# Performance work log

Hardware: AMD Instinct MI355X
Metric: run time of the kernel (lower is better)

The kernel has to match this reference:

```python
import jax, jax.numpy as jnp
import numpy as np

N = 100000      # nodes
D = 128         # in_channels
P = 64          # num_prompts
E = 3_200_000   # graph edges
EPT = 5_000_000 # kNN prompt-graph edges (k=50)
EPS = 0.1       # ot_epsilon
ITERS = 20      # sinkhorn max_iters


def _l2norm(x):
    # F.normalize(p=2, dim=1) with eps=1e-12
    return x / jnp.maximum(jnp.linalg.norm(x, axis=1, keepdims=True), 1e-12)


def setup_inputs() -> dict:
    key = jax.random.key(0)
    k1, k2, k3, k4, k5 = jax.random.split(key, 5)
    x = jax.random.normal(k1, (N, D), dtype=jnp.float32)
    edge_index = jax.random.randint(k2, (2, E), 0, N, dtype=jnp.int32)
    edge_weight = jax.random.uniform(k3, (E,), dtype=jnp.float32)
    pt_edge_index = jax.random.randint(k4, (2, EPT), 0, N, dtype=jnp.int32)
    # xavier_uniform for prompt_tokens
    bound = float(np.sqrt(6.0 / (P + D)))
    prompt_tokens = jax.random.uniform(k5, (P, D), dtype=jnp.float32, minval=-bound, maxval=bound)
    alpha_feat = jnp.float32(0.01)
    gamma = jnp.float32(0.5)
    return {"x": x, "edge_index": edge_index, "edge_weight": edge_weight,
            "pt_edge_index": pt_edge_index, "prompt_tokens": prompt_tokens,
            "alpha_feat": alpha_feat, "gamma": gamma}


def reference(x, edge_index, edge_weight, pt_edge_index, prompt_tokens, alpha_feat, gamma):
    n = x.shape[0]
    row, col = edge_index[0], edge_index[1]
    # degree of col (unweighted count), GCN-style symmetric normalization
    deg = jax.ops.segment_sum(jnp.ones_like(edge_weight), col, num_segments=n)
    deg_inv_sqrt = jnp.where(deg > 0, deg ** -0.5, 0.0)
    norm_weight = deg_inv_sqrt[row] * edge_weight * deg_inv_sqrt[col]  # [E]
    # scatter-add aggregation: x_aggr[row] += x[col] * norm_weight
    x_aggr = jax.ops.segment_sum(x[col] * norm_weight[:, None], row, num_segments=n)
    x_struct = (1.0 - gamma) * x + gamma * x_aggr

    xs = _l2norm(x_struct)               # [N, D]
    pn = _l2norm(prompt_tokens)          # [P, D]

    # Sinkhorn OT: cost = 1 - cosine sim, uniform marginals
    C = 1.0 - xs @ pn.T                  # [N, P]
    K = jnp.exp(-C / EPS)
    p = prompt_tokens.shape[0]
    a = jnp.full((n,), 1.0 / n, dtype=x.dtype)
    b = jnp.full((p,), 1.0 / p, dtype=x.dtype)
    u = a
    for _ in range(ITERS):
        v = b / (K.T @ u + 1e-30)
        u = a / (K @ v + 1e-30)
    T_star = u[:, None] * K * v[None, :]  # [N, P]
    ot_loss = jnp.sum(T_star * C)

    prompt_message = n * (T_star @ prompt_tokens)  # [N, D]
    x_adapted = x + alpha_feat * prompt_message

    xf = _l2norm(x_adapted)
    pt_row, pt_col = pt_edge_index[0], pt_edge_index[1]
    w = jnp.sum(xf[pt_row] * xf[pt_col], axis=1)   # [EPT]
    w = jax.nn.relu(w)
    w = w / (jnp.max(w) + 1e-8)
    return (x_adapted, ot_loss, w)
```

## Files before the change

kernel.cpp:

```cpp
#include <hip/hip_runtime.h>
#include <stdint.h>

#define D_DIM 128
#define P_DIM 64

#define O_CNTR   0x000000ull
#define O_CNTC   0x080000ull
#define O_DIS    0x100000ull
#define O_ROWPTR 0x180000ull
#define O_CURSOR 0x200000ull
#define O_PART   0x280000ull
#define O_KT     0x290000ull
#define O_MAXW   0x2A0000ull
#define O_PNB    0x2B0000ull
#define O_U      0x300000ull
#define O_CSR    0x400000ull
#define O_XF     0x400000ull
#define O_K      0x1C80000ull
#define O_XB     0x3580000ull

__device__ __forceinline__ float wsumf(float v){
  #pragma unroll
  for (int d=1; d<64; d<<=1) v += __shfl_xor(v, d);
  return v;
}

__device__ __forceinline__ unsigned f2bf(float f){
  unsigned u = __float_as_uint(f);
  return (u + 0x7fffu + ((u>>16)&1u)) >> 16;
}

__device__ __forceinline__ float bflo(unsigned u){ return __uint_as_float(u<<16); }
__device__ __forceinline__ float bfhi(unsigned u){ return __uint_as_float(u & 0xffff0000u); }

__device__ __forceinline__ float dp2(unsigned a, unsigned b){
  return bflo(a)*bflo(b) + bfhi(a)*bfhi(b);
}

__global__ void k_zero(int* cntr, int* cntc, float* kt, unsigned* maxw, float* loss_slot, int n){
  int i = blockIdx.x*blockDim.x + threadIdx.x;
  int st = gridDim.x*blockDim.x;
  for (int j=i; j<n; j+=st){ cntr[j]=0; cntc[j]=0; }
  for (int j=i; j<21*64; j+=st) kt[j]=0.f;
  if (i==0){ *maxw = 0u; *loss_slot = 0.f; }
}

__global__ void k_deg(const int* __restrict__ ei, int E, int* cntr, int* cntc){
  int i = blockIdx.x*blockDim.x + threadIdx.x;
  int st = gridDim.x*blockDim.x;
  for (int e=i; e<E; e+=st){
    atomicAdd(&cntr[ei[e]], 1);
    atomicAdd(&cntc[ei[E+e]], 1);
  }
}

__global__ void k_deginv(const int* __restrict__ cntc, float* __restrict__ dis, int n){
  int i = blockIdx.x*blockDim.x + threadIdx.x;
  if (i < n){
    int c = cntc[i];
    dis[i] = (c > 0) ? rsqrtf((float)c) : 0.f;
  }
}

__global__ void k_prep_x(const float* __restrict__ x, unsigned* __restrict__ xb, int n64){
  int i = blockIdx.x*blockDim.x + threadIdx.x;
  int st = gridDim.x*blockDim.x;
  for (int j=i; j<n64; j+=st){
    float2 v = ((const float2*)x)[j];
    xb[j] = f2bf(v.x) | (f2bf(v.y)<<16);
  }
}

__global__ void k_scan_a(const int* __restrict__ cnt, int* __restrict__ part, int n){
  __shared__ int sm[4];
  int base = blockIdx.x*1024;
  int t = threadIdx.x;
  int s = 0;
  #pragma unroll
  for (int k=0;k<4;k++){ int idx = base + t + 256*k; if (idx<n) s += cnt[idx]; }
  #pragma unroll
  for (int d=1; d<64; d<<=1) s += __shfl_xor(s, d);
  if ((t&63)==0) sm[t>>6] = s;
  __syncthreads();
  if (t==0) part[blockIdx.x] = sm[0]+sm[1]+sm[2]+sm[3];
}

__global__ void k_scan_b(int* part, int nb, int* row_ptr, int n, int E){
  if (threadIdx.x==0 && blockIdx.x==0){
    int run = 0;
    for (int i=0;i<nb;i++){ int v = part[i]; part[i] = run; run += v; }
    row_ptr[n] = E;
  }
}

__global__ void k_scan_c(const int* __restrict__ cnt, const int* __restrict__ part,
                         int* __restrict__ row_ptr, int* __restrict__ cursor, int n){
  __shared__ int warp_tot[4];
  int base = blockIdx.x*1024;
  int t = threadIdx.x;
  int lane = t&63, wv = t>>6;
  int v[4];
  #pragma unroll
  for (int k=0;k<4;k++){ int idx = base + t*4 + k; v[k] = (idx<n) ? cnt[idx] : 0; }
  int local = v[0]+v[1]+v[2]+v[3];
  int sc = local;
  #pragma unroll
  for (int d=1; d<64; d<<=1){ int y = __shfl_up(sc, d); if (lane>=d) sc += y; }
  if (lane==63) warp_tot[wv] = sc;
  __syncthreads();
  int woff = 0;
  for (int i=0;i<wv;i++) woff += warp_tot[i];
  int run = part[blockIdx.x] + woff + (sc - local);
  #pragma unroll
  for (int k=0;k<4;k++){
    int idx = base + t*4 + k;
    if (idx<n){ row_ptr[idx] = run; cursor[idx] = run; run += v[k]; }
  }
}

__global__ void k_prep_pn(const float* __restrict__ pt, unsigned* __restrict__ pnb){
  int r = blockIdx.x;
  int l = threadIdx.x;
  float2 v = ((const float2*)pt)[r*64 + l];
  float ss = wsumf(v.x*v.x + v.y*v.y);
  float inv = 1.f / fmaxf(sqrtf(ss), 1e-12f);
  pnb[l*64 + r] = f2bf(v.x*inv) | (f2bf(v.y*inv) << 16);
}

__global__ void k_scatter(const int* __restrict__ ei, const float* __restrict__ ew,
                          const float* __restrict__ dis, int* cursor,
                          uint2* __restrict__ csr, int E){
  int i = blockIdx.x*blockDim.x + threadIdx.x;
  int st = gridDim.x*blockDim.x;
  for (int e=i; e<E; e+=st){
    int r = ei[e], c = ei[E+e];
    float w = dis[r]*ew[e]*dis[c];
    int pos = atomicAdd(&cursor[r], 1);
    csr[pos] = make_uint2((unsigned)c, __float_as_uint(w));
  }
}

__global__ __launch_bounds__(256) void k_struct(const float* __restrict__ x,
    const unsigned* __restrict__ xb,
    const int* __restrict__ row_ptr, const uint2* __restrict__ csr,
    const unsigned* __restrict__ pnb_g, const float* __restrict__ gamma_p,
    float* __restrict__ Km, float* __restrict__ kt0, int n){
  __shared__ unsigned pnbs[64*64];
  __shared__ __align__(16) float xsrow[4][128];
  __shared__ float ktsh[64];
  int tid = threadIdx.x;
  for (int i=tid; i<4096; i+=256) pnbs[i] = pnb_g[i];
  if (tid<64) ktsh[tid] = 0.f;
  __syncthreads();
  float g = *gamma_p, om = 1.f - g;
  int lane = tid&63, wv = tid>>6;
  int wid = blockIdx.x*4 + wv, nw = gridDim.x*4;
  const float2* X2 = (const float2*)x;
  float kacc = 0.f;
  for (int r=wid; r<n; r+=nw){
    int e0 = row_ptr[r], e1 = row_ptr[r+1];
    float ax=0.f, ay=0.f;
    int e = e0;
    for (; e+7 < e1; e += 8){
      uint2 q0 = csr[e],   q1 = csr[e+1], q2 = csr[e+2], q3 = csr[e+3];
      uint2 q4 = csr[e+4], q5 = csr[e+5], q6 = csr[e+6], q7 = csr[e+7];
      unsigned b0 = xb[(size_t)q0.x*64 + lane];
      unsigned b1 = xb[(size_t)q1.x*64 + lane];
      unsigned b2 = xb[(size_t)q2.x*64 + lane];
      unsigned b3 = xb[(size_t)q3.x*64 + lane];
      unsigned b4 = xb[(size_t)q4.x*64 + lane];
      unsigned b5 = xb[(size_t)q5.x*64 + lane];
      unsigned b6 = xb[(size_t)q6.x*64 + lane];
      unsigned b7 = xb[(size_t)q7.x*64 + lane];
      float w0 = __uint_as_float(q0.y), w1 = __uint_as_float(q1.y);
      float w2 = __uint_as_float(q2.y), w3 = __uint_as_float(q3.y);
      float w4 = __uint_as_float(q4.y), w5 = __uint_as_float(q5.y);
      float w6 = __uint_as_float(q6.y), w7 = __uint_as_float(q7.y);
      ax = fmaf(w0, bflo(b0), ax); ay = fmaf(w0, bfhi(b0), ay);
      ax = fmaf(w1, bflo(b1), ax); ay = fmaf(w1, bfhi(b1), ay);
      ax = fmaf(w2, bflo(b2), ax); ay = fmaf(w2, bfhi(b2), ay);
      ax = fmaf(w3, bflo(b3), ax); ay = fmaf(w3, bfhi(b3), ay);
      ax = fmaf(w4, bflo(b4), ax); ay = fmaf(w4, bfhi(b4), ay);
      ax = fmaf(w5, bflo(b5), ax); ay = fmaf(w5, bfhi(b5), ay);
      ax = fmaf(w6, bflo(b6), ax); ay = fmaf(w6, bfhi(b6), ay);
      ax = fmaf(w7, bflo(b7), ax); ay = fmaf(w7, bfhi(b7), ay);
    }
    for (; e < e1; e++){
      uint2 q = csr[e];
      unsigned b = xb[(size_t)q.x*64 + lane];
      float w = __uint_as_float(q.y);
      ax = fmaf(w, bflo(b), ax); ay = fmaf(w, bfhi(b), ay);
    }
    float2 xr = X2[(size_t)r*64 + lane];
    float sx = om*xr.x + g*ax;
    float sy = om*xr.y + g*ay;
    float ss = wsumf(sx*sx + sy*sy);
    float inv = 1.f / fmaxf(sqrtf(ss), 1e-12f);
    xsrow[wv][2*lane]   = sx*inv;
    xsrow[wv][2*lane+1] = sy*inv;
    float acc = 0.f;
    #pragma unroll
    for (int k=0; k<64; k++){
      unsigned pp = pnbs[k*64 + lane];
      float2 xv = *(const float2*)&xsrow[wv][2*k];
      acc = fmaf(bflo(pp), xv.x, acc);
      acc = fmaf(bfhi(pp), xv.y, acc);
    }
    float kv = exp2f((acc - 1.f) * 14.426950408889634f);
    Km[(size_t)r*64 + lane] = kv;
    kacc += kv;
  }
  atomicAdd(&ktsh[lane], kacc);
  __syncthreads();
  if (tid<64) atomicAdd(&kt0[tid], ktsh[tid] * (1.0f/(float)n));
}

__global__ __launch_bounds__(256) void k_sink(const float* __restrict__ Km,
    const float* __restrict__ kt_in, float* __restrict__ kt_out,
    float* __restrict__ u, int n){
  __shared__ __align__(16) float vsh[64];
  __shared__ float ktsh[64];
  int tid = threadIdx.x;
  if (tid<64){ vsh[tid] = (1.0f/64.0f)/(kt_in[tid] + 1e-30f); ktsh[tid] = 0.f; }
  __syncthreads();
  int lane = tid&63, wv = tid>>6, sub = lane>>4, li = lane&15;
  float4 vv = ((const float4*)vsh)[li];
  float anorm = 1.0f/(float)n;
  float4 acc = make_float4(0,0,0,0);
  int xcd = blockIdx.x & 7, lb = blockIdx.x >> 3, nlb = gridDim.x >> 3;
  int r0 = (int)((long long)xcd*n/8), r1 = (int)((long long)(xcd+1)*n/8);
  int wid = lb*4 + wv, nw = nlb*4;
  for (int base=r0+wid*4; base<r1; base+=nw*4){
    int r = base + sub;
    float4 kv = make_float4(0,0,0,0);
    if (r<r1) kv = ((const float4*)(Km + (size_t)r*64))[li];
    float d = kv.x*vv.x + kv.y*vv.y + kv.z*vv.z + kv.w*vv.w;
    d += __shfl_xor(d,1); d += __shfl_xor(d,2); d += __shfl_xor(d,4); d += __shfl_xor(d,8);
    float un = anorm/(d + 1e-30f);
    if (li==0 && r<r1) u[r] = un;
    acc.x = fmaf(kv.x, un, acc.x);
    acc.y = fmaf(kv.y, un, acc.y);
    acc.z = fmaf(kv.z, un, acc.z);
    acc.w = fmaf(kv.w, un, acc.w);
  }
  acc.x += __shfl_xor(acc.x,16); acc.x += __shfl_xor(acc.x,32);
  acc.y += __shfl_xor(acc.y,16); acc.y += __shfl_xor(acc.y,32);
  acc.z += __shfl_xor(acc.z,16); acc.z += __shfl_xor(acc.z,32);
  acc.w += __shfl_xor(acc.w,16); acc.w += __shfl_xor(acc.w,32);
  if (sub==0){
    atomicAdd(&ktsh[li*4+0], acc.x);
    atomicAdd(&ktsh[li*4+1], acc.y);
    atomicAdd(&ktsh[li*4+2], acc.z);
    atomicAdd(&ktsh[li*4+3], acc.w);
  }
  __syncthreads();
  if (tid<64) atomicAdd(&kt_out[tid], ktsh[tid]);
}

__global__ __launch_bounds__(256) void k_final(const float* __restrict__ x,
    const float* __restrict__ Km, const float* __restrict__ u,
    const float* __restrict__ kt19, const float* __restrict__ pt,
    const float* __restrict__ alpha_p, float* __restrict__ out_x,
    float* __restrict__ out_loss, unsigned* __restrict__ xf, int n){
  __shared__ __align__(16) float pts[64*128];
  __shared__ float trow[4][64];
  __shared__ float vsh[64];
  __shared__ float blockloss;
  int tid = threadIdx.x;
  for (int i=tid; i<8192; i+=256) pts[i] = pt[i];
  if (tid<64) vsh[tid] = (1.0f/64.0f)/(kt19[tid] + 1e-30f);
  if (tid==0) blockloss = 0.f;
  __syncthreads();
  float alpha = *alpha_p;
  float coeff = alpha*(float)n;
  int lane = tid&63, wv = tid>>6;
  int xcd = blockIdx.x & 7, lb = blockIdx.x >> 3, nlb = gridDim.x >> 3;
  int r0 = (int)((long long)xcd*n/8), r1 = (int)((long long)(xcd+1)*n/8);
  int wid = lb*4 + wv, nw = nlb*4;
  float lossacc = 0.f;
  for (int r=r0+wid; r<r1; r+=nw){
    float kv = Km[(size_t)r*64 + lane];
    float T = u[r]*kv*vsh[lane];
    float C = log2f(kv) * (-0.069314718055994531f);
    lossacc = fmaf(T, C, lossacc);
    trow[wv][lane] = T;
    float m0=0.f, m1=0.f;
    #pragma unroll
    for (int p=0; p<64; p++){
      float t = trow[wv][p];
      float2 pv = ((const float2*)pts)[p*64 + lane];
      m0 = fmaf(t, pv.x, m0); m1 = fmaf(t, pv.y, m1);
    }
    float2 xr = ((const float2*)x)[(size_t)r*64 + lane];
    float ox = fmaf(coeff, m0, xr.x);
    float oy = fmaf(coeff, m1, xr.y);
    ((float2*)out_x)[(size_t)r*64 + lane] = make_float2(ox, oy);
    float ss = wsumf(ox*ox + oy*oy);
    float inv = 1.f / fmaxf(sqrtf(ss), 1e-12f);
    unsigned lo = f2bf(ox*inv), hi = f2bf(oy*inv);
    xf[(size_t)r*64 + lane] = lo | (hi<<16);
  }
  lossacc = wsumf(lossacc);
  if (lane==0) atomicAdd(&blockloss, lossacc);
  __syncthreads();
  if (tid==0) atomicAdd(out_loss, blockloss);
}

__global__ __launch_bounds__(256) void k_edge(const int* __restrict__ pte,
    const unsigned* __restrict__ xf, float* __restrict__ wout,
    unsigned* __restrict__ maxw, int ept){
  __shared__ unsigned blockmax;
  if (threadIdx.x==0) blockmax = 0u;
  __syncthreads();
  int lane = threadIdx.x&63, wv = threadIdx.x>>6, sub = lane>>4, li = lane&15;
  int wid = blockIdx.x*4 + wv, nw = gridDim.x*4;
  float lm = 0.f;
  for (int base=wid*16; base<ept; base+=nw*16){
    int ej[4]; bool vj[4]; int rj[4], cj[4];
    uint4 Aj[4], Bj[4];
    float dj[4];
    #pragma unroll
    for (int j=0;j<4;j++){ ej[j] = base + 4*j + sub; vj[j] = ej[j] < ept; }
    #pragma unroll
    for (int j=0;j<4;j++){
      rj[j] = vj[j] ? pte[ej[j]] : 0;
      cj[j] = vj[j] ? pte[ept+ej[j]] : 0;
    }
    #pragma unroll
    for (int j=0;j<4;j++){
      Aj[j] = *(((const uint4*)(xf + (size_t)rj[j]*64)) + li);
      Bj[j] = *(((const uint4*)(xf + (size_t)cj[j]*64)) + li);
    }
    #pragma unroll
    for (int j=0;j<4;j++){
      dj[j] = dp2(Aj[j].x,Bj[j].x) + dp2(Aj[j].y,Bj[j].y)
            + dp2(Aj[j].z,Bj[j].z) + dp2(Aj[j].w,Bj[j].w);
      dj[j] += __shfl_xor(dj[j],1); dj[j] += __shfl_xor(dj[j],2);
      dj[j] += __shfl_xor(dj[j],4); dj[j] += __shfl_xor(dj[j],8);
    }
    if (li==0){
      #pragma unroll
      for (int j=0;j<4;j++){
        if (vj[j]){ float w = fmaxf(dj[j], 0.f); wout[ej[j]] = w; lm = fmaxf(lm, w); }
      }
    }
  }
  #pragma unroll
  for (int d=1; d<64; d<<=1) lm = fmaxf(lm, __shfl_xor(lm, d));
  if (lane==0) atomicMax(&blockmax, __float_as_uint(lm));
  __syncthreads();
  if (threadIdx.x==0) atomicMax(maxw, blockmax);
}

__global__ void k_normw(float* __restrict__ w, const unsigned* __restrict__ maxw, int ept){
  float inv = 1.f/(__uint_as_float(*maxw) + 1e-8f);
  int i = blockIdx.x*blockDim.x + threadIdx.x;
  int st = gridDim.x*blockDim.x;
  for (int e=i; e<ept; e+=st) w[e] *= inv;
}

extern "C" void kernel_launch(void* const* d_in, const int* in_sizes, int n_in,
                              void* d_out, int out_size, void* d_ws, size_t ws_size,
                              hipStream_t stream){
  const float* x       = (const float*)d_in[0];
  const int*   ei      = (const int*)  d_in[1];
  const float* ew      = (const float*)d_in[2];
  const int*   pte     = (const int*)  d_in[3];
  const float* pt      = (const float*)d_in[4];
  const float* alpha_p = (const float*)d_in[5];
  const float* gamma_p = (const float*)d_in[6];
  int n   = in_sizes[0] / D_DIM;
  int E   = in_sizes[1] / 2;
  int ept = in_sizes[3] / 2;

  char* ws = (char*)d_ws;
  int*      cntr    = (int*)     (ws + O_CNTR);
  int*      cntc    = (int*)     (ws + O_CNTC);
  float*    dis     = (float*)   (ws + O_DIS);
  int*      row_ptr = (int*)     (ws + O_ROWPTR);
  int*      cursor  = (int*)     (ws + O_CURSOR);
  int*      part    = (int*)     (ws + O_PART);
  float*    kt      = (float*)   (ws + O_KT);
  unsigned* maxw    = (unsigned*)(ws + O_MAXW);
  unsigned* pnb     = (unsigned*)(ws + O_PNB);
  float*    ubuf    = (float*)   (ws + O_U);
  uint2*    csr     = (uint2*)   (ws + O_CSR);
  unsigned* xf      = (unsigned*)(ws + O_XF);
  float*    Km      = (float*)   (ws + O_K);
  unsigned* xb      = (unsigned*)(ws + O_XB);

  float* out_x    = (float*)d_out;
  float* out_loss = (float*)d_out + (size_t)n*D_DIM;
  float* out_w    = out_loss + 1;

  int nb = (n + 1023)/1024;

  k_zero   <<<512, 256, 0, stream>>>(cntr, cntc, kt, maxw, out_loss, n);
  k_deg    <<<2048, 256, 0, stream>>>(ei, E, cntr, cntc);
  k_deginv <<<(n+255)/256, 256, 0, stream>>>(cntc, dis, n);
  k_prep_x <<<2048, 256, 0, stream>>>(x, xb, n*64);
  k_scan_a <<<nb, 256, 0, stream>>>(cntr, part, n);
  k_scan_b <<<1, 64, 0, stream>>>(part, nb, row_ptr, n, E);
  k_scan_c <<<nb, 256, 0, stream>>>(cntr, part, row_ptr, cursor, n);
  k_prep_pn<<<64, 64, 0, stream>>>(pt, pnb);
  k_scatter<<<2048, 256, 0, stream>>>(ei, ew, dis, cursor, csr, E);
  k_struct <<<1024, 256, 0, stream>>>(x, xb, row_ptr, csr, pnb, gamma_p, Km, kt, n);
  for (int t=1; t<=20; t++)
    k_sink <<<1024, 256, 0, stream>>>(Km, kt + (t-1)*64, kt + t*64, ubuf, n);
  k_final  <<<1024, 256, 0, stream>>>(x, Km, ubuf, kt + 19*64, pt, alpha_p,
                                      out_x, out_loss, xf, n);
  k_edge   <<<2048, 256, 0, stream>>>(pte, xf, out_w, maxw, ept);
  k_normw  <<<2048, 256, 0, stream>>>(out_w, maxw, ept);
}
```

Measured before the change: 1.851 ms.

## Fuse struct, Sinkhorn iterations and final pass into one cooperative register-resident kernel

Replaces the struct kernel, the 20 Sinkhorn launches and the final kernel with one cooperative kernel. Each wave keeps its 25 rows of K in registers across iterations and uses grid.sync instead of separate launches. This avoids re-reading the 25.6 MB K matrix from memory on every iteration and removes per-launch overhead. The costs are high register pressure, since the grid must fit 1024x256 threads co-resident to cover all rows, and a grid-wide barrier on every iteration; if the cooperative launch fails, the code falls back to the old kernel sequence.

```diff
diff --git a/kernel.cpp b/kernel.cpp
--- a/kernel.cpp
+++ b/kernel.cpp
@@ -1,8 +1,12 @@
 #include <hip/hip_runtime.h>
+#include <hip/hip_cooperative_groups.h>
 #include <stdint.h>
+
+namespace cg = cooperative_groups;
 
 #define D_DIM 128
 #define P_DIM 64
+#define KR 25
 
 #define O_CNTR   0x000000ull
 #define O_CNTC   0x080000ull
@@ -140,6 +144,156 @@
   }
 }
 
+__device__ __forceinline__ void row_aggregate(int r, int lane, float om, float g,
+    const float2* __restrict__ X2, const unsigned* __restrict__ xb,
+    const int* __restrict__ row_ptr, const uint2* __restrict__ csr,
+    float* __restrict__ xsr ){
+  int e0 = row_ptr[r], e1 = row_ptr[r+1];
+  float ax=0.f, ay=0.f;
+  int e = e0;
+  for (; e+7 < e1; e += 8){
+    uint2 q0 = csr[e],   q1 = csr[e+1], q2 = csr[e+2], q3 = csr[e+3];
+    uint2 q4 = csr[e+4], q5 = csr[e+5], q6 = csr[e+6], q7 = csr[e+7];
+    unsigned b0 = xb[(size_t)q0.x*64 + lane];
+    unsigned b1 = xb[(size_t)q1.x*64 + lane];
+    unsigned b2 = xb[(size_t)q2.x*64 + lane];
+    unsigned b3 = xb[(size_t)q3.x*64 + lane];
+    unsigned b4 = xb[(size_t)q4.x*64 + lane];
+    unsigned b5 = xb[(size_t)q5.x*64 + lane];
+    unsigned b6 = xb[(size_t)q6.x*64 + lane];
+    unsigned b7 = xb[(size_t)q7.x*64 + lane];
+    float w0 = __uint_as_float(q0.y), w1 = __uint_as_float(q1.y);
+    float w2 = __uint_as_float(q2.y), w3 = __uint_as_float(q3.y);
+    float w4 = __uint_as_float(q4.y), w5 = __uint_as_float(q5.y);
+    float w6 = __uint_as_float(q6.y), w7 = __uint_as_float(q7.y);
+    ax = fmaf(w0, bflo(b0), ax); ay = fmaf(w0, bfhi(b0), ay);
+    ax = fmaf(w1, bflo(b1), ax); ay = fmaf(w1, bfhi(b1), ay);
+    ax = fmaf(w2, bflo(b2), ax); ay = fmaf(w2, bfhi(b2), ay);
+    ax = fmaf(w3, bflo(b3), ax); ay = fmaf(w3, bfhi(b3), ay);
+    ax = fmaf(w4, bflo(b4), ax); ay = fmaf(w4, bfhi(b4), ay);
+    ax = fmaf(w5, bflo(b5), ax); ay = fmaf(w5, bfhi(b5), ay);
+    ax = fmaf(w6, bflo(b6), ax); ay = fmaf(w6, bfhi(b6), ay);
+    ax = fmaf(w7, bflo(b7), ax); ay = fmaf(w7, bfhi(b7), ay);
+  }
+  for (; e < e1; e++){
+    uint2 q = csr[e];
+    unsigned b = xb[(size_t)q.x*64 + lane];
+    float w = __uint_as_float(q.y);
+    ax = fmaf(w, bflo(b), ax); ay = fmaf(w, bfhi(b), ay);
+  }
+  float2 xr = X2[(size_t)r*64 + lane];
+  float sx = om*xr.x + g*ax;
+  float sy = om*xr.y + g*ay;
+  float ss = wsumf(sx*sx + sy*sy);
+  float inv = 1.f / fmaxf(sqrtf(ss), 1e-12f);
+  xsr[2*lane]   = sx*inv;
+  xsr[2*lane+1] = sy*inv;
+}
+
+__global__ __launch_bounds__(256, 4) void k_mega(
+    const float* __restrict__ x, const unsigned* __restrict__ xb,
+    const int* __restrict__ row_ptr, const uint2* __restrict__ csr,
+    const unsigned* __restrict__ pnb, const float* __restrict__ pt,
+    const float* __restrict__ gamma_p, const float* __restrict__ alpha_p,
+    float* __restrict__ kt, float* __restrict__ out_x, float* __restrict__ out_loss,
+    unsigned* __restrict__ xf, int n){
+  __shared__ __align__(16) float xsrow[4][128];
+  __shared__ float ktsh[64];
+  __shared__ float blockloss;
+  cg::grid_group grid = cg::this_grid();
+  int tid = threadIdx.x, lane = tid&63, wv = tid>>6;
+  if (tid<64) ktsh[tid] = 0.f;
+  if (tid==0) blockloss = 0.f;
+  __syncthreads();
+  float g = *gamma_p, om = 1.f - g;
+  float anorm = 1.0f/(float)n;
+  int wid = blockIdx.x*4 + wv;
+  int r0 = wid*KR;
+  const float2* X2 = (const float2*)x;
+  float K[KR];
+  float kacc = 0.f;
+
+  #pragma unroll
+  for (int i=0; i<KR; i++){
+    K[i] = 0.f;
+    int r = r0 + i;
+    if (r < n){
+      row_aggregate(r, lane, om, g, X2, xb, row_ptr, csr, xsrow[wv]);
+      float acc = 0.f;
+      #pragma unroll
+      for (int k=0; k<64; k++){
+        unsigned pp = pnb[k*64 + lane];
+        float2 xv = *(const float2*)&xsrow[wv][2*k];
+        acc = fmaf(bflo(pp), xv.x, acc);
+        acc = fmaf(bfhi(pp), xv.y, acc);
+      }
+      K[i] = exp2f((acc - 1.f) * 14.426950408889634f);
+      kacc += K[i];
+    }
+  }
+  atomicAdd(&ktsh[lane], kacc);
+  __syncthreads();
+  if (tid<64) atomicAdd(&kt[tid], ktsh[tid] * anorm);
+  grid.sync();
+
+  for (int t=1; t<=19; t++){
+    float vl = 0.015625f / (kt[(t-1)*64 + lane] + 1e-30f);
+    if (tid<64) ktsh[tid] = 0.f;
+    __syncthreads();
+    float colacc = 0.f;
+    #pragma unroll
+    for (int i=0; i<KR; i++){
+      int r = r0 + i;
+      if (r < n){
+        float d = wsumf(K[i]*vl);
+        float ur = anorm / (d + 1e-30f);
+        colacc = fmaf(K[i], ur, colacc);
+      }
+    }
+    atomicAdd(&ktsh[lane], colacc);
+    __syncthreads();
+    if (tid<64) atomicAdd(&kt[t*64 + tid], ktsh[tid]);
+    grid.sync();
+  }
+
+  float vl = 0.015625f / (kt[19*64 + lane] + 1e-30f);
+  float coeff = (*alpha_p) * (float)n;
+  float lossacc = 0.f;
+  const float2* PT2 = (const float2*)pt;
+  #pragma unroll
+  for (int i=0; i<KR; i++){
+    int r = r0 + i;
+    if (r < n){
+      float kv = K[i];
+      float d = wsumf(kv*vl);
+      float ur = anorm / (d + 1e-30f);
+      float Tl = ur * kv * vl;
+      float Cl = log2f(kv) * (-0.069314718055994531f);
+      lossacc = fmaf(Tl, Cl, lossacc);
+      xsrow[wv][lane] = Tl;
+      float m0=0.f, m1=0.f;
+      #pragma unroll
+      for (int p=0; p<64; p++){
+        float tP = xsrow[wv][p];
+        float2 pv = PT2[p*64 + lane];
+        m0 = fmaf(tP, pv.x, m0);
+        m1 = fmaf(tP, pv.y, m1);
+      }
+      float2 xr = X2[(size_t)r*64 + lane];
+      float ox = fmaf(coeff, m0, xr.x);
+      float oy = fmaf(coeff, m1, xr.y);
+      ((float2*)out_x)[(size_t)r*64 + lane] = make_float2(ox, oy);
+      float ss = wsumf(ox*ox + oy*oy);
+      float inv = 1.f / fmaxf(sqrtf(ss), 1e-12f);
+      xf[(size_t)r*64 + lane] = f2bf(ox*inv) | (f2bf(oy*inv)<<16);
+    }
+  }
+  lossacc = wsumf(lossacc);
+  if (lane==0) atomicAdd(&blockloss, lossacc);
+  __syncthreads();
+  if (tid==0) atomicAdd(out_loss, blockloss);
+}
+
 __global__ __launch_bounds__(256) void k_struct(const float* __restrict__ x,
     const unsigned* __restrict__ xb,
     const int* __restrict__ row_ptr, const uint2* __restrict__ csr,
@@ -158,46 +312,7 @@
   const float2* X2 = (const float2*)x;
   float kacc = 0.f;
   for (int r=wid; r<n; r+=nw){
-    int e0 = row_ptr[r], e1 = row_ptr[r+1];
-    float ax=0.f, ay=0.f;
-    int e = e0;
-    for (; e+7 < e1; e += 8){
-      uint2 q0 = csr[e],   q1 = csr[e+1], q2 = csr[e+2], q3 = csr[e+3];
-      uint2 q4 = csr[e+4], q5 = csr[e+5], q6 = csr[e+6], q7 = csr[e+7];
-      unsigned b0 = xb[(size_t)q0.x*64 + lane];
-      unsigned b1 = xb[(size_t)q1.x*64 + lane];
-      unsigned b2 = xb[(size_t)q2.x*64 + lane];
-      unsigned b3 = xb[(size_t)q3.x*64 + lane];
-      unsigned b4 = xb[(size_t)q4.x*64 + lane];
-      unsigned b5 = xb[(size_t)q5.x*64 + lane];
-      unsigned b6 = xb[(size_t)q6.x*64 + lane];
-      unsigned b7 = xb[(size_t)q7.x*64 + lane];
-      float w0 = __uint_as_float(q0.y), w1 = __uint_as_float(q1.y);
-      float w2 = __uint_as_float(q2.y), w3 = __uint_as_float(q3.y);
-      float w4 = __uint_as_float(q4.y), w5 = __uint_as_float(q5.y);
-      float w6 = __uint_as_float(q6.y), w7 = __uint_as_float(q7.y);
-      ax = fmaf(w0, bflo(b0), ax); ay = fmaf(w0, bfhi(b0), ay);
-      ax = fmaf(w1, bflo(b1), ax); ay = fmaf(w1, bfhi(b1), ay);
-      ax = fmaf(w2, bflo(b2), ax); ay = fmaf(w2, bfhi(b2), ay);
-      ax = fmaf(w3, bflo(b3), ax); ay = fmaf(w3, bfhi(b3), ay);
-      ax = fmaf(w4, bflo(b4), ax); ay = fmaf(w4, bfhi(b4), ay);
-      ax = fmaf(w5, bflo(b5), ax); ay = fmaf(w5, bfhi(b5), ay);
-      ax = fmaf(w6, bflo(b6), ax); ay = fmaf(w6, bfhi(b6), ay);
-      ax = fmaf(w7, bflo(b7), ax); ay = fmaf(w7, bfhi(b7), ay);
-    }
-    for (; e < e1; e++){
-      uint2 q = csr[e];
-      unsigned b = xb[(size_t)q.x*64 + lane];
-      float w = __uint_as_float(q.y);
-      ax = fmaf(w, bflo(b), ax); ay = fmaf(w, bfhi(b), ay);
-    }
-    float2 xr = X2[(size_t)r*64 + lane];
-    float sx = om*xr.x + g*ax;
-    float sy = om*xr.y + g*ay;
-    float ss = wsumf(sx*sx + sy*sy);
-    float inv = 1.f / fmaxf(sqrtf(ss), 1e-12f);
-    xsrow[wv][2*lane]   = sx*inv;
-    xsrow[wv][2*lane+1] = sy*inv;
+    row_aggregate(r, lane, om, g, X2, xb, row_ptr, csr, xsrow[wv]);
     float acc = 0.f;
     #pragma unroll
     for (int k=0; k<64; k++){
@@ -297,8 +412,7 @@
     ((float2*)out_x)[(size_t)r*64 + lane] = make_float2(ox, oy);
     float ss = wsumf(ox*ox + oy*oy);
     float inv = 1.f / fmaxf(sqrtf(ss), 1e-12f);
-    unsigned lo = f2bf(ox*inv), hi = f2bf(oy*inv);
-    xf[(size_t)r*64 + lane] = lo | (hi<<16);
+    xf[(size_t)r*64 + lane] = f2bf(ox*inv) | (f2bf(oy*inv)<<16);
   }
   lossacc = wsumf(lossacc);
   if (lane==0) atomicAdd(&blockloss, lossacc);
@@ -404,11 +518,25 @@
   k_scan_c <<<nb, 256, 0, stream>>>(cntr, part, row_ptr, cursor, n);
   k_prep_pn<<<64, 64, 0, stream>>>(pt, pnb);
   k_scatter<<<2048, 256, 0, stream>>>(ei, ew, dis, cursor, csr, E);
-  k_struct <<<1024, 256, 0, stream>>>(x, xb, row_ptr, csr, pnb, gamma_p, Km, kt, n);
-  for (int t=1; t<=20; t++)
-    k_sink <<<1024, 256, 0, stream>>>(Km, kt + (t-1)*64, kt + t*64, ubuf, n);
-  k_final  <<<1024, 256, 0, stream>>>(x, Km, ubuf, kt + 19*64, pt, alpha_p,
-                                      out_x, out_loss, xf, n);
+
+  hipError_t coop_st;
+  {
+    void* args[] = {
+      (void*)&x, (void*)&xb, (void*)&row_ptr, (void*)&csr, (void*)&pnb, (void*)&pt,
+      (void*)&gamma_p, (void*)&alpha_p, (void*)&kt, (void*)&out_x, (void*)&out_loss,
+      (void*)&xf, (void*)&n
+    };
+    coop_st = hipLaunchCooperativeKernel((void*)k_mega, dim3(1024), dim3(256),
+                                         args, 0, stream);
+  }
+  if (coop_st != hipSuccess){
+    k_struct <<<1024, 256, 0, stream>>>(x, xb, row_ptr, csr, pnb, gamma_p, Km, kt, n);
+    for (int t=1; t<=20; t++)
+      k_sink <<<1024, 256, 0, stream>>>(Km, kt + (t-1)*64, kt + t*64, ubuf, n);
+    k_final  <<<1024, 256, 0, stream>>>(x, Km, ubuf, kt + 19*64, pt, alpha_p,
+                                        out_x, out_loss, xf, n);
+  }
+
   k_edge   <<<2048, 256, 0, stream>>>(pte, xf, out_w, maxw, ept);
   k_normw  <<<2048, 256, 0, stream>>>(out_w, maxw, ept);
 }
```

New measurement: 4.100 ms. 2.22x slower.
